# Kernel optimization log

Hardware: AMD Instinct MI355X
Metric: run time of the kernel (lower is better)

The kernel has to match this reference:

```python
import jax, jax.numpy as jnp
import numpy as np

D = 256        # feature dim
H = 8          # num_heads
HD = D // H    # head dim = 32
G = 16         # graphs in batch
NA = 128       # nodes per graph, side A
NB = 128       # nodes per graph, side B


def setup_inputs() -> dict:
    key = jax.random.key(0)
    ks = jax.random.split(key, 7)
    s = 1.0 / np.sqrt(D)
    A = jax.random.normal(ks[0], (G * NA, D), dtype=jnp.float32)
    B = jax.random.normal(ks[1], (G * NB, D), dtype=jnp.float32)
    batch1 = jnp.repeat(jnp.arange(G, dtype=jnp.int64), NA)
    batch2 = jnp.repeat(jnp.arange(G, dtype=jnp.int64), NB)
    W1 = jax.random.normal(ks[2], (D, D), dtype=jnp.float32) * s
    bias1 = jax.random.normal(ks[3], (D,), dtype=jnp.float32) * s
    W2 = jax.random.normal(ks[4], (D, D), dtype=jnp.float32) * s
    bias2 = jax.random.normal(ks[5], (D,), dtype=jnp.float32) * s
    q = jax.random.normal(ks[6], (HD,), dtype=jnp.float32) * s
    return {"A": A, "batch1": batch1, "B": B, "batch2": batch2,
            "W1": W1, "bias1": bias1, "W2": W2, "bias2": bias2, "q": q}


def reference(A, batch1, B, batch2, W1, bias1, W2, bias2, q):
    # equal-size graphs: counts are uniform, so torch.split == reshape
    g = int(np.asarray(batch1)[-1]) + 1
    nA = A.shape[0] // g
    nB = B.shape[0] // g
    x1 = A @ W1.T + bias1            # [g*nA, D]
    x2 = B @ W2.T + bias2            # [g*nB, D]
    # faithful to torch: raw C-order view [nA, D] -> [H, nA, HD]
    x1 = x1.reshape(g, H, nA, HD)    # [g, H, nA, hd]
    x2 = x2.reshape(g, H, nB, HD)    # [g, H, nB, hd]
    # att[g,h,i,j] = sum_k tanh(x1[g,h,i,k] * x2[g,h,j,k]) * q[k]
    att = jnp.einsum('ghijk,k->ghij',
                     jnp.tanh(x1[:, :, :, None, :] * x2[:, :, None, :, :]), q)
    b2a = jax.nn.softmax(att.mean(axis=3), axis=2)   # [g, H, nA]
    a2b = jax.nn.softmax(att.mean(axis=2), axis=2)   # [g, H, nB]
    A_p = jnp.einsum('ghik,ghi->ghk', x1, b2a).reshape(g, D)
    B_p = jnp.einsum('ghjk,ghj->ghk', x2, a2b).reshape(g, D)
    return jnp.concatenate([A_p, B_p], axis=1)       # [g, 2D]
```

## Files before the change

### kernel.cpp

```cpp
#include <hip/hip_runtime.h>

#define C2L2E 2.8853900817779268f
#define LOG2E 1.4426950408889634f

#define WS_X1  0
#define WS_X2  524288
#define WS_RS  1048576
#define WS_CP  1064960

#define L_SMAT 0
#define L_COLP 8448
#define L_RED8 8960
#define L_X2   9216
#define L_X1   13312

__device__ __forceinline__ int swz4(int row, int c4) { return (c4 ^ (row & 7)) << 2; }

__global__ __launch_bounds__(256) void k1_gemm(
        const float* __restrict__ A, const float* __restrict__ B,
        const float* __restrict__ W1, const float* __restrict__ b1,
        const float* __restrict__ W2, const float* __restrict__ b2,
        float* __restrict__ ws) {
    __shared__ float At[2][32 * 36];
    __shared__ float Wt[2][32 * 68];
    const int tid = threadIdx.x, bid = blockIdx.x;
    const int idx = bid & 255, mat = bid >> 8;
    const int r0 = (idx >> 2) * 32, c0 = (idx & 3) * 64;
    const float* In = mat ? B : A;
    const float* W  = mat ? W2 : W1;
    const float* bs = mat ? b2 : b1;
    float* xo = ws + (mat ? WS_X2 : WS_X1);

    const int tm = tid & 7, tn = tid >> 3;
    const int arow = tid >> 3, akq = tid & 7;

    float acc[4][2];
    #pragma unroll
    for (int i = 0; i < 4; ++i) { acc[i][0] = 0.f; acc[i][1] = 0.f; }

    {
        float4 av = *(const float4*)(In + (size_t)(r0 + arow) * 256 + akq * 4);
        At[0][(akq*4+0)*36 + arow] = av.x;
        At[0][(akq*4+1)*36 + arow] = av.y;
        At[0][(akq*4+2)*36 + arow] = av.z;
        At[0][(akq*4+3)*36 + arow] = av.w;
        float4 w0 = *(const float4*)(W + (size_t)(c0 + arow) * 256 + akq * 4);
        Wt[0][(akq*4+0)*68 + arow] = w0.x;
        Wt[0][(akq*4+1)*68 + arow] = w0.y;
        Wt[0][(akq*4+2)*68 + arow] = w0.z;
        Wt[0][(akq*4+3)*68 + arow] = w0.w;
        float4 w1v = *(const float4*)(W + (size_t)(c0 + 32 + arow) * 256 + akq * 4);
        Wt[0][(akq*4+0)*68 + 32 + arow] = w1v.x;
        Wt[0][(akq*4+1)*68 + 32 + arow] = w1v.y;
        Wt[0][(akq*4+2)*68 + 32 + arow] = w1v.z;
        Wt[0][(akq*4+3)*68 + 32 + arow] = w1v.w;
    }
    __syncthreads();

    for (int kt = 0; kt < 8; ++kt) {
        const int b = kt & 1;
        float4 av, w0, w1v;
        if (kt < 7) {
            av  = *(const float4*)(In + (size_t)(r0 + arow) * 256 + (kt+1)*32 + akq * 4);
            w0  = *(const float4*)(W + (size_t)(c0 + arow) * 256 + (kt+1)*32 + akq * 4);
            w1v = *(const float4*)(W + (size_t)(c0 + 32 + arow) * 256 + (kt+1)*32 + akq * 4);
        }
        #pragma unroll
        for (int k = 0; k < 32; ++k) {
            float4 a4 = *(const float4*)(&At[b][k*36 + tm*4]);
            float2 w2 = *(const float2*)(&Wt[b][k*68 + tn*2]);
            acc[0][0] = fmaf(a4.x, w2.x, acc[0][0]);
            acc[0][1] = fmaf(a4.x, w2.y, acc[0][1]);
            acc[1][0] = fmaf(a4.y, w2.x, acc[1][0]);
            acc[1][1] = fmaf(a4.y, w2.y, acc[1][1]);
            acc[2][0] = fmaf(a4.z, w2.x, acc[2][0]);
            acc[2][1] = fmaf(a4.z, w2.y, acc[2][1]);
            acc[3][0] = fmaf(a4.w, w2.x, acc[3][0]);
            acc[3][1] = fmaf(a4.w, w2.y, acc[3][1]);
        }
        if (kt < 7) {
            const int nb = b ^ 1;
            At[nb][(akq*4+0)*36 + arow] = av.x;
            At[nb][(akq*4+1)*36 + arow] = av.y;
            At[nb][(akq*4+2)*36 + arow] = av.z;
            At[nb][(akq*4+3)*36 + arow] = av.w;
            Wt[nb][(akq*4+0)*68 + arow] = w0.x;
            Wt[nb][(akq*4+1)*68 + arow] = w0.y;
            Wt[nb][(akq*4+2)*68 + arow] = w0.z;
            Wt[nb][(akq*4+3)*68 + arow] = w0.w;
            Wt[nb][(akq*4+0)*68 + 32 + arow] = w1v.x;
            Wt[nb][(akq*4+1)*68 + 32 + arow] = w1v.y;
            Wt[nb][(akq*4+2)*68 + 32 + arow] = w1v.z;
            Wt[nb][(akq*4+3)*68 + 32 + arow] = w1v.w;
            __syncthreads();
        }
    }

    const float2 bv = *(const float2*)(bs + c0 + tn * 2);
    #pragma unroll
    for (int i = 0; i < 4; ++i) {
        float2 o; o.x = acc[i][0] + bv.x; o.y = acc[i][1] + bv.y;
        *(float2*)(xo + (size_t)(r0 + tm*4 + i) * 256 + c0 + tn * 2) = o;
    }
}

__global__ __launch_bounds__(512) void k2_att(
        float* __restrict__ ws, const float* __restrict__ q) {
    __shared__ float sm[15360];
    const int tid = threadIdx.x;
    const int gh = blockIdx.x >> 1, s = blockIdx.x & 1;
    float* x2L = sm + L_X2;
    float* x1L = sm + L_X1;

    {
        const float4* src2 = (const float4*)(ws + WS_X2 + (size_t)gh * 4096);
        #pragma unroll
        for (int p = 0; p < 2; ++p) {
            int n = tid + p * 512;
            float4 v = src2[n];
            int ni = n >> 3, c4 = n & 7;
            *(float4*)(x2L + ni * 32 + swz4(ni, c4)) = v;
        }
        const float4* src1 = (const float4*)(ws + WS_X1 + (size_t)gh * 4096 + s * 2048);
        float4 v = src1[tid];
        int nl = tid >> 3, c4 = tid & 7;
        *(float4*)(x1L + nl * 32 + swz4(nl, c4)) = v;
    }
    __syncthreads();

    {
        const int j = tid & 127, iset = tid >> 7;
        float xr[32], qt[32];
        #pragma unroll
        for (int cc = 0; cc < 8; ++cc) {
            float4 v = *(float4*)(x2L + j * 32 + swz4(j, cc));
            xr[cc*4+0] = v.x * C2L2E; xr[cc*4+1] = v.y * C2L2E;
            xr[cc*4+2] = v.z * C2L2E; xr[cc*4+3] = v.w * C2L2E;
            float4 qv = *(const float4*)(q + cc * 4);
            qt[cc*4+0] = -2.f * qv.x; qt[cc*4+1] = -2.f * qv.y;
            qt[cc*4+2] = -2.f * qv.z; qt[cc*4+3] = -2.f * qv.w;
        }
        float colacc = 0.f;
        for (int rr = 0; rr < 16; ++rr) {
            const int r = iset * 16 + rr;
            float a[32];
            #pragma unroll
            for (int cc = 0; cc < 8; ++cc) {
                float4 v = *(float4*)(x1L + r * 32 + swz4(r, cc));
                a[cc*4+0] = v.x; a[cc*4+1] = v.y; a[cc*4+2] = v.z; a[cc*4+3] = v.w;
            }
            float S0 = 0.f, S1 = 0.f;
            #pragma unroll
            for (int kp = 0; kp < 16; ++kp) {
                float p0 = a[2*kp]   * xr[2*kp];
                float p1 = a[2*kp+1] * xr[2*kp+1];
                float d0 = __builtin_amdgcn_exp2f(fminf(p0, 60.f)) + 1.f;
                float d1 = __builtin_amdgcn_exp2f(fminf(p1, 60.f)) + 1.f;
                float rD = __builtin_amdgcn_rcpf(d0 * d1);
                float U  = fmaf(qt[2*kp+1], d0, qt[2*kp] * d1);
                if (kp & 1) S1 = fmaf(U, rD, S1); else S0 = fmaf(U, rD, S0);
            }
            float S = S0 + S1;
            colacc += S;
            sm[L_SMAT + r * 132 + j] = S;
        }
        sm[L_COLP + iset * 128 + j] = colacc;
    }
    __syncthreads();

    if (tid < 256) {
        const int row = tid >> 2, seg = tid & 3;
        float acc = 0.f;
        #pragma unroll
        for (int m = 0; m < 8; ++m) {
            float4 v = *(float4*)(sm + L_SMAT + row * 132 + seg * 32 + m * 4);
            acc += (v.x + v.y) + (v.z + v.w);
        }
        sm[L_RED8 + row * 4 + seg] = acc;
    }
    __syncthreads();
    if (tid < 64) {
        float v = sm[L_RED8 + tid*4] + sm[L_RED8 + tid*4+1]
                + sm[L_RED8 + tid*4+2] + sm[L_RED8 + tid*4+3];
        ws[WS_RS + gh * 128 + s * 64 + tid] = v;
    } else if (tid < 192) {
        const int j = tid - 64;
        ws[WS_CP + (size_t)(gh * 2 + s) * 128 + j] =
            sm[L_COLP + j] + sm[L_COLP + 128 + j] + sm[L_COLP + 256 + j] + sm[L_COLP + 384 + j];
    }
}

__global__ __launch_bounds__(256) void kb_finish(
        const float* __restrict__ ws, float* __restrict__ out) {
    const int gh = blockIdx.x;
    const int g = gh >> 3, h = gh & 7;
    const int tid = threadIdx.x;
    const int side = tid >> 7;
    const int u = tid & 127;
    const int w2 = (u >> 6) & 1;
    const int lane = tid & 63;

    __shared__ float warr[2][128];
    __shared__ float red[4];
    __shared__ float red2[4];
    __shared__ float part[2][4][32];

    float m;
    if (side == 0) {
        m = ws[WS_RS + gh * 128 + u] * 0.0078125f;
    } else {
        m = (ws[WS_CP + (size_t)(gh * 2 + 0) * 128 + u] +
             ws[WS_CP + (size_t)(gh * 2 + 1) * 128 + u]) * 0.0078125f;
    }

    float mx = m;
    #pragma unroll
    for (int d = 32; d >= 1; d >>= 1) mx = fmaxf(mx, __shfl_xor(mx, d));
    if (lane == 0) red[side * 2 + w2] = mx;
    __syncthreads();
    mx = fmaxf(red[side * 2], red[side * 2 + 1]);

    float e = __builtin_amdgcn_exp2f((m - mx) * LOG2E);
    float sme = e;
    #pragma unroll
    for (int d = 32; d >= 1; d >>= 1) sme += __shfl_xor(sme, d);
    if (lane == 0) red2[side * 2 + w2] = sme;
    __syncthreads();
    const float tot = red2[side * 2] + red2[side * 2 + 1];
    warr[side][u] = e * __builtin_amdgcn_rcpf(tot);
    __syncthreads();

    const int k = u & 31, is = u >> 5;
    const float* xt = ws + (side ? WS_X2 : WS_X1) + (size_t)gh * 4096;
    float p = 0.f;
    #pragma unroll 4
    for (int r = 0; r < 32; ++r)
        p = fmaf(xt[(is * 32 + r) * 32 + k], warr[side][is * 32 + r], p);
    part[side][is][k] = p;
    __syncthreads();
    if (u < 32 && side == 0) {
        float o = part[0][0][u] + part[0][1][u] + part[0][2][u] + part[0][3][u];
        out[(size_t)g * 512 + h * 32 + u] = o;
    } else if (u < 32 && side == 1) {
        float o = part[1][0][u] + part[1][1][u] + part[1][2][u] + part[1][3][u];
        out[(size_t)g * 512 + 256 + h * 32 + u] = o;
    }
}

extern "C" void kernel_launch(void* const* d_in, const int* in_sizes, int n_in,
                              void* d_out, int out_size, void* d_ws, size_t ws_size,
                              hipStream_t stream) {
    const float* A  = (const float*)d_in[0];
    const float* B  = (const float*)d_in[2];
    const float* W1 = (const float*)d_in[4];
    const float* b1 = (const float*)d_in[5];
    const float* W2 = (const float*)d_in[6];
    const float* b2 = (const float*)d_in[7];
    const float* q  = (const float*)d_in[8];
    float* ws  = (float*)d_ws;
    float* out = (float*)d_out;

    k1_gemm<<<512, 256, 0, stream>>>(A, B, W1, b1, W2, b2, ws);
    k2_att<<<256, 512, 0, stream>>>(ws, q);
    kb_finish<<<128, 256, 0, stream>>>(ws, out);
}
```

Baseline: 41.81 us.

## Replace FP32 SIMT projection GEMM with split-bf16 MFMA plus conversion pre-pass

Adds a pre-pass kernel that splits A, B, W1 and W2 into high and low bf16 parts in workspace. The projection GEMM then runs on 16x16x32 bf16 MFMA instructions, using three products (hi*hi, hi*lo, lo*hi) to approximate fp32 accuracy. Operands are read directly from global memory with no LDS staging. This trades scalar FMA throughput for matrix-core throughput, at the cost of an extra kernel launch, extra global traffic for the converted copies, and a slight loss of precision.

```diff
diff --git a/kernel.cpp b/kernel.cpp
--- a/kernel.cpp
+++ b/kernel.cpp
@@ -3,10 +3,18 @@
 #define C2L2E 2.8853900817779268f
 #define LOG2E 1.4426950408889634f
 
-#define WS_X1  0
-#define WS_X2  524288
-#define WS_RS  1048576
-#define WS_CP  1064960
+#define WS_X1   0
+#define WS_X2   524288
+#define WS_RS   1048576
+#define WS_CP   1064960
+#define WS_AH   1114112
+#define WS_AL   1376256
+#define WS_BH   1638400
+#define WS_BL   1900544
+#define WS_W1H  2162688
+#define WS_W1L  2195456
+#define WS_W2H  2228224
+#define WS_W2L  2260992
 
 #define L_SMAT 0
 #define L_COLP 8448
@@ -14,93 +22,86 @@
 #define L_X2   9216
 #define L_X1   13312
 
+typedef short bf16x8 __attribute__((ext_vector_type(8)));
+typedef float f32x4 __attribute__((ext_vector_type(4)));
+
 __device__ __forceinline__ int swz4(int row, int c4) { return (c4 ^ (row & 7)) << 2; }
 
-__global__ __launch_bounds__(256) void k1_gemm(
+__device__ __forceinline__ unsigned short bf16rne(float f) {
+    unsigned u = __float_as_uint(f);
+    u += 0x7FFF + ((u >> 16) & 1);
+    return (unsigned short)(u >> 16);
+}
+__device__ __forceinline__ float bf16tof(unsigned short h) {
+    return __uint_as_float(((unsigned)h) << 16);
+}
+
+__global__ __launch_bounds__(512) void k0_convert(
         const float* __restrict__ A, const float* __restrict__ B,
-        const float* __restrict__ W1, const float* __restrict__ b1,
-        const float* __restrict__ W2, const float* __restrict__ b2,
+        const float* __restrict__ W1, const float* __restrict__ W2,
         float* __restrict__ ws) {
-    __shared__ float At[2][32 * 36];
-    __shared__ float Wt[2][32 * 68];
-    const int tid = threadIdx.x, bid = blockIdx.x;
-    const int idx = bid & 255, mat = bid >> 8;
-    const int r0 = (idx >> 2) * 32, c0 = (idx & 3) * 64;
-    const float* In = mat ? B : A;
-    const float* W  = mat ? W2 : W1;
+    const int idx = blockIdx.x * 512 + threadIdx.x;
+    const float* src; unsigned short *dh, *dl; int base;
+    if (idx < 131072)      { src = A;  dh = (unsigned short*)(ws + WS_AH);  dl = (unsigned short*)(ws + WS_AL);  base = idx; }
+    else if (idx < 262144) { src = B;  dh = (unsigned short*)(ws + WS_BH);  dl = (unsigned short*)(ws + WS_BL);  base = idx - 131072; }
+    else if (idx < 278528) { src = W1; dh = (unsigned short*)(ws + WS_W1H); dl = (unsigned short*)(ws + WS_W1L); base = idx - 262144; }
+    else                   { src = W2; dh = (unsigned short*)(ws + WS_W2H); dl = (unsigned short*)(ws + WS_W2L); base = idx - 278528; }
+    float4 v = ((const float4*)src)[base];
+    ushort4 h, l;
+    h.x = bf16rne(v.x); l.x = bf16rne(v.x - bf16tof(h.x));
+    h.y = bf16rne(v.y); l.y = bf16rne(v.y - bf16tof(h.y));
+    h.z = bf16rne(v.z); l.z = bf16rne(v.z - bf16tof(h.z));
+    h.w = bf16rne(v.w); l.w = bf16rne(v.w - bf16tof(h.w));
+    ((ushort4*)dh)[base] = h;
+    ((ushort4*)dl)[base] = l;
+}
+
+__global__ __launch_bounds__(256) void k1_mfma(
+        const float* __restrict__ b1, const float* __restrict__ b2,
+        float* __restrict__ ws) {
+    const int bid = blockIdx.x, tid = threadIdx.x;
+    const int mat = bid >> 7, idx = bid & 127;
+    const int r0 = (idx >> 2) * 64, c0 = (idx & 3) * 64;
+    const unsigned short* IH = (const unsigned short*)(ws + (mat ? WS_BH : WS_AH));
+    const unsigned short* IL = (const unsigned short*)(ws + (mat ? WS_BL : WS_AL));
+    const unsigned short* WH = (const unsigned short*)(ws + (mat ? WS_W2H : WS_W1H));
+    const unsigned short* WL = (const unsigned short*)(ws + (mat ? WS_W2L : WS_W1L));
     const float* bs = mat ? b2 : b1;
     float* xo = ws + (mat ? WS_X2 : WS_X1);
 
-    const int tm = tid & 7, tn = tid >> 3;
-    const int arow = tid >> 3, akq = tid & 7;
-
-    float acc[4][2];
-    #pragma unroll
-    for (int i = 0; i < 4; ++i) { acc[i][0] = 0.f; acc[i][1] = 0.f; }
-
-    {
-        float4 av = *(const float4*)(In + (size_t)(r0 + arow) * 256 + akq * 4);
-        At[0][(akq*4+0)*36 + arow] = av.x;
-        At[0][(akq*4+1)*36 + arow] = av.y;
-        At[0][(akq*4+2)*36 + arow] = av.z;
-        At[0][(akq*4+3)*36 + arow] = av.w;
-        float4 w0 = *(const float4*)(W + (size_t)(c0 + arow) * 256 + akq * 4);
-        Wt[0][(akq*4+0)*68 + arow] = w0.x;
-        Wt[0][(akq*4+1)*68 + arow] = w0.y;
-        Wt[0][(akq*4+2)*68 + arow] = w0.z;
-        Wt[0][(akq*4+3)*68 + arow] = w0.w;
-        float4 w1v = *(const float4*)(W + (size_t)(c0 + 32 + arow) * 256 + akq * 4);
-        Wt[0][(akq*4+0)*68 + 32 + arow] = w1v.x;
-        Wt[0][(akq*4+1)*68 + 32 + arow] = w1v.y;
-        Wt[0][(akq*4+2)*68 + 32 + arow] = w1v.z;
-        Wt[0][(akq*4+3)*68 + 32 + arow] = w1v.w;
-    }
-    __syncthreads();
+    const int wv = tid >> 6, lane = tid & 63;
+    const int l16 = lane & 15, khi = (lane >> 4) * 8;
+    const int row = r0 + wv * 16 + l16;
+
+    f32x4 acc[4];
+    #pragma unroll
+    for (int nt = 0; nt < 4; ++nt) acc[nt] = (f32x4){0.f, 0.f, 0.f, 0.f};
+
+    const unsigned short* ihp = IH + (size_t)row * 256 + khi;
+    const unsigned short* ilp = IL + (size_t)row * 256 + khi;
 
     for (int kt = 0; kt < 8; ++kt) {
-        const int b = kt & 1;
-        float4 av, w0, w1v;
-        if (kt < 7) {
-            av  = *(const float4*)(In + (size_t)(r0 + arow) * 256 + (kt+1)*32 + akq * 4);
-            w0  = *(const float4*)(W + (size_t)(c0 + arow) * 256 + (kt+1)*32 + akq * 4);
-            w1v = *(const float4*)(W + (size_t)(c0 + 32 + arow) * 256 + (kt+1)*32 + akq * 4);
-        }
-        #pragma unroll
-        for (int k = 0; k < 32; ++k) {
-            float4 a4 = *(const float4*)(&At[b][k*36 + tm*4]);
-            float2 w2 = *(const float2*)(&Wt[b][k*68 + tn*2]);
-            acc[0][0] = fmaf(a4.x, w2.x, acc[0][0]);
-            acc[0][1] = fmaf(a4.x, w2.y, acc[0][1]);
-            acc[1][0] = fmaf(a4.y, w2.x, acc[1][0]);
-            acc[1][1] = fmaf(a4.y, w2.y, acc[1][1]);
-            acc[2][0] = fmaf(a4.z, w2.x, acc[2][0]);
-            acc[2][1] = fmaf(a4.z, w2.y, acc[2][1]);
-            acc[3][0] = fmaf(a4.w, w2.x, acc[3][0]);
-            acc[3][1] = fmaf(a4.w, w2.y, acc[3][1]);
-        }
-        if (kt < 7) {
-            const int nb = b ^ 1;
-            At[nb][(akq*4+0)*36 + arow] = av.x;
-            At[nb][(akq*4+1)*36 + arow] = av.y;
-            At[nb][(akq*4+2)*36 + arow] = av.z;
-            At[nb][(akq*4+3)*36 + arow] = av.w;
-            Wt[nb][(akq*4+0)*68 + arow] = w0.x;
-            Wt[nb][(akq*4+1)*68 + arow] = w0.y;
-            Wt[nb][(akq*4+2)*68 + arow] = w0.z;
-            Wt[nb][(akq*4+3)*68 + arow] = w0.w;
-            Wt[nb][(akq*4+0)*68 + 32 + arow] = w1v.x;
-            Wt[nb][(akq*4+1)*68 + 32 + arow] = w1v.y;
-            Wt[nb][(akq*4+2)*68 + 32 + arow] = w1v.z;
-            Wt[nb][(akq*4+3)*68 + 32 + arow] = w1v.w;
-            __syncthreads();
-        }
-    }
-
-    const float2 bv = *(const float2*)(bs + c0 + tn * 2);
-    #pragma unroll
-    for (int i = 0; i < 4; ++i) {
-        float2 o; o.x = acc[i][0] + bv.x; o.y = acc[i][1] + bv.y;
-        *(float2*)(xo + (size_t)(r0 + tm*4 + i) * 256 + c0 + tn * 2) = o;
+        bf16x8 ah = *(const bf16x8*)(ihp + kt * 32);
+        bf16x8 al = *(const bf16x8*)(ilp + kt * 32);
+        #pragma unroll
+        for (int nt = 0; nt < 4; ++nt) {
+            const int cB = c0 + nt * 16 + l16;
+            bf16x8 wh = *(const bf16x8*)(WH + (size_t)cB * 256 + kt * 32 + khi);
+            bf16x8 wl = *(const bf16x8*)(WL + (size_t)cB * 256 + kt * 32 + khi);
+            acc[nt] = __builtin_amdgcn_mfma_f32_16x16x32_bf16(ah, wh, acc[nt], 0, 0, 0);
+            acc[nt] = __builtin_amdgcn_mfma_f32_16x16x32_bf16(ah, wl, acc[nt], 0, 0, 0);
+            acc[nt] = __builtin_amdgcn_mfma_f32_16x16x32_bf16(al, wh, acc[nt], 0, 0, 0);
+        }
+    }
+
+    const int rowb = r0 + wv * 16 + (lane >> 4) * 4;
+    #pragma unroll
+    for (int nt = 0; nt < 4; ++nt) {
+        const int col = c0 + nt * 16 + l16;
+        const float bb = bs[col];
+        #pragma unroll
+        for (int rg = 0; rg < 4; ++rg)
+            xo[(size_t)(rowb + rg) * 256 + col] = acc[nt][rg] + bb;
     }
 }
 
@@ -260,7 +261,8 @@
     float* ws  = (float*)d_ws;
     float* out = (float*)d_out;
 
-    k1_gemm<<<512, 256, 0, stream>>>(A, B, W1, b1, W2, b2, ws);
+    k0_convert<<<576, 512, 0, stream>>>(A, B, W1, W2, ws);
+    k1_mfma<<<256, 256, 0, stream>>>(b1, b2, ws);
     k2_att<<<256, 512, 0, stream>>>(ws, q);
     kb_finish<<<128, 256, 0, stream>>>(ws, out);
 }
```

Result: slower. 45.38 us (+8.5%).
